# Kernel optimization log

Hardware: AMD Instinct MI355X
Metric: run time of the kernel (lower is better)

## Reference

```python
import jax, jax.numpy as jnp
import numpy as np

K = 512
H = 8
B = 8
T = 1024
EPS = 1e-5


def _layernorm(x, g, b):
    mu = jnp.mean(x, axis=-1, keepdims=True)
    var = jnp.var(x, axis=-1, keepdims=True)
    return (x - mu) * jax.lax.rsqrt(var + EPS) * g + b


def _attention(x, enc, wq, wk, wv, wo):
    b, t, k = x.shape
    h = H
    scale = k ** (-0.25)
    q = (x @ wq).reshape(b, t, h, k) * scale        # [b,t,h,k]
    kk = (enc @ wk).reshape(b, t, h, k) * scale
    v = (enc @ wv).reshape(b, t, h, k)
    dot = jnp.einsum('bqhd,bkhd->bhqk', q, kk)      # [b,h,t,t]
    att = jax.nn.softmax(dot, axis=-1)
    out = jnp.einsum('bhqk,bkhd->bqhd', att, v).reshape(b, t, h * k)
    return out @ wo                                  # [b,t,k]


def setup_inputs() -> dict:
    key = jax.random.key(0)
    ks = jax.random.split(key, 12)
    s = 0.02
    return {
        'x': jax.random.normal(ks[0], (B, T, K), jnp.float32),
        'enc': jax.random.normal(ks[1], (B, T, K), jnp.float32),
        'sa_wq': jax.random.normal(ks[2], (K, K * H), jnp.float32) * s,
        'sa_wk': jax.random.normal(ks[3], (K, K * H), jnp.float32) * s,
        'sa_wv': jax.random.normal(ks[4], (K, K * H), jnp.float32) * s,
        'sa_wo': jax.random.normal(ks[5], (K * H, K), jnp.float32) * s,
        'ca_wq': jax.random.normal(ks[6], (K, K * H), jnp.float32) * s,
        'ca_wk': jax.random.normal(ks[7], (K, K * H), jnp.float32) * s,
        'ca_wv': jax.random.normal(ks[8], (K, K * H), jnp.float32) * s,
        'ca_wo': jax.random.normal(ks[9], (K * H, K), jnp.float32) * s,
        'ln1_g': jnp.ones((K,), jnp.float32), 'ln1_b': jnp.zeros((K,), jnp.float32),
        'ln2_g': jnp.ones((K,), jnp.float32), 'ln2_b': jnp.zeros((K,), jnp.float32),
        'ln3_g': jnp.ones((K,), jnp.float32), 'ln3_b': jnp.zeros((K,), jnp.float32),
        'ff_w1': jax.random.normal(ks[10], (K, 4 * K), jnp.float32) * s,
        'ff_b1': jnp.zeros((4 * K,), jnp.float32),
        'ff_w2': jax.random.normal(ks[11], (4 * K, K), jnp.float32) * s,
        'ff_b2': jnp.zeros((K,), jnp.float32),
    }


def reference(x, enc, sa_wq, sa_wk, sa_wv, sa_wo, ca_wq, ca_wk, ca_wv, ca_wo,
              ln1_g, ln1_b, ln2_g, ln2_b, ln3_g, ln3_b,
              ff_w1, ff_b1, ff_w2, ff_b2):
    # masked self-attention (mask_future_steps=False -> plain self-attn)
    sa = _attention(x, x, sa_wq, sa_wk, sa_wv, sa_wo)
    x = _layernorm(sa + x, ln1_g, ln1_b)
    # encoder-decoder attention
    ca = _attention(x, enc, ca_wq, ca_wk, ca_wv, ca_wo)
    x = _layernorm(ca + x, ln2_g, ln2_b)
    # dropout p=0.0 -> identity
    ff = jax.nn.relu(x @ ff_w1 + ff_b1) @ ff_w2 + ff_b2
    x = _layernorm(ff + x, ln3_g, ln3_b)
    return x
```

## Files before the change

kernel.cpp:

```cpp
#include <hip/hip_runtime.h>
#include <stdint.h>

typedef short short8 __attribute__((ext_vector_type(8)));
typedef float f32x4 __attribute__((ext_vector_type(4)));
typedef unsigned short us4 __attribute__((ext_vector_type(4)));

#define DEVI static __device__ __forceinline__

DEVI float b2f(unsigned short u) {
  union { float f; uint32_t i; } v; v.i = ((uint32_t)u) << 16; return v.f;
}
DEVI unsigned short f2b(float f) {
  union { float f; uint32_t i; } v; v.f = f;
  uint32_t r = v.i + 0x7FFFu + ((v.i >> 16) & 1u);
  return (unsigned short)(r >> 16);
}

DEVI void async_cp16(const unsigned short* g, unsigned short* l) {
  __builtin_amdgcn_global_load_lds(
      (const __attribute__((address_space(1))) void*)g,
      (__attribute__((address_space(3))) void*)l, 16, 0, 0);
}

DEVI void swz(int& bx, int& by, int& bz) {
  const int gx = gridDim.x, gy = gridDim.y, gz = gridDim.z;
  int l = blockIdx.x + gx * (blockIdx.y + gy * blockIdx.z);
  bz = l % gz; l /= gz;
  by = l % gy;
  bx = l / gy;
}


__global__ __launch_bounds__(256) void cvt_f32_bf16(
    const float4* __restrict__ src, unsigned short* __restrict__ dst) {
  const int i = blockIdx.x * 256 + threadIdx.x;
  float4 f = src[i];
  uint2 o;
  o.x = (uint32_t)f2b(f.x) | ((uint32_t)f2b(f.y) << 16);
  o.y = (uint32_t)f2b(f.z) | ((uint32_t)f2b(f.w) << 16);
  ((uint2*)dst)[i] = o;
}

__global__ __launch_bounds__(256) void wtrans(
    const float* __restrict__ src, unsigned short* __restrict__ dst, int R, int C) {
  __shared__ float tile[32][33];
  const int tx = threadIdx.x & 31, ty = threadIdx.x >> 5;
  const int c0 = blockIdx.x * 32, r0 = blockIdx.y * 32;
#pragma unroll
  for (int i = 0; i < 32; i += 8)
    tile[ty + i][tx] = src[(long)(r0 + ty + i) * C + c0 + tx];
  __syncthreads();
#pragma unroll
  for (int i = 0; i < 32; i += 8)
    dst[(long)(c0 + ty + i) * R + r0 + tx] = f2b(tile[tx][ty + i]);
}

__global__ __launch_bounds__(256) void layernorm_rows(
    const float* X, const float* __restrict__ g,
    const float* __restrict__ b, float* Y,
    unsigned short* __restrict__ Yb) {
  const int tid = threadIdx.x;
  const long row = blockIdx.x;
  const float* x = X + row * 512;
  float v0 = x[tid], v1 = x[tid + 256];
  float s1 = v0 + v1;
  float s2 = v0 * v0 + v1 * v1;
#pragma unroll
  for (int o = 1; o < 64; o <<= 1) {
    s1 += __shfl_xor(s1, o);
    s2 += __shfl_xor(s2, o);
  }
  __shared__ float r1[4], r2[4];
  const int lane = tid & 63, wave = tid >> 6;
  if (lane == 0) { r1[wave] = s1; r2[wave] = s2; }
  __syncthreads();
  s1 = r1[0] + r1[1] + r1[2] + r1[3];
  s2 = r2[0] + r2[1] + r2[2] + r2[3];
  const float mu = s1 * (1.f / 512.f);
  const float var = s2 * (1.f / 512.f) - mu * mu;
  const float rs = rsqrtf(var + 1e-5f);
  float y0 = (v0 - mu) * rs * g[tid] + b[tid];
  float y1 = (v1 - mu) * rs * g[tid + 256] + b[tid + 256];
  if (Y) { Y[row * 512 + tid] = y0; Y[row * 512 + tid + 256] = y1; }
  if (Yb) { Yb[row * 512 + tid] = f2b(y0); Yb[row * 512 + tid + 256] = f2b(y1); }
}

template <int EPI, int BM, int BK, int SMAX = 0>
__global__ __launch_bounds__(256, 2) void gemm_bt(
    const unsigned short* __restrict__ A, int lda, long asb, long ash,
    const unsigned short* __restrict__ B, int ldb, long bsb, long bsh,
    void* Cv, int ldc, long csb, long csh,
    int K, float scale,
    const float* __restrict__ bias, const float* res) {
  constexpr int MI = BM / 32;
  constexpr int KS = BK / 32;
  constexpr int CPR = BK / 8;
  constexpr int SWM = CPR - 1;
  constexpr int RPL = (BK >= 64) ? 1 : (64 / BK);
  static_assert(!SMAX || (BM == 128 && EPI == 0), "SMAX: BM=128, EPI=0 only");
  __shared__ __align__(16) unsigned short As[2][BM * BK];
  __shared__ __align__(16) unsigned short Bs[2][128 * BK];
  __shared__ float inv_s[SMAX ? 128 : 1];
  int bx, by, bz;
  swz(bx, by, bz);
  const int tid = threadIdx.x;
  const int lane = tid & 63;
  const int wave = tid >> 6;
  const int zb = bz >> 3, zh = bz & 7;
  const int m0 = by * BM;
  const int n0 = bx * 128;

  const unsigned short* Ab = A + zb * asb + zh * ash + (long)m0 * lda;
  const unsigned short* Bb = B + zb * bsb + zh * bsh + (long)n0 * ldb;

  if constexpr (SMAX) {
    unsigned short* Sp = (unsigned short*)Ab;
    const int g16 = tid & 15;
#pragma unroll
    for (int p = 0; p < 8; p++) {
      const int r = p * 16 + (tid >> 4);
      us4* rowp = (us4*)(Sp + (long)r * lda);
      us4 raw[16];
#pragma unroll
      for (int c = 0; c < 16; c++) raw[c] = rowp[g16 + c * 16];
      float m = -3.0e38f;
#pragma unroll
      for (int c = 0; c < 16; c++)
#pragma unroll
        for (int e = 0; e < 4; e++) m = fmaxf(m, b2f(raw[c][e]));
#pragma unroll
      for (int o = 1; o < 16; o <<= 1) m = fmaxf(m, __shfl_xor(m, o));
      float s = 0.f;
#pragma unroll
      for (int c = 0; c < 16; c++) {
        us4 outv;
#pragma unroll
        for (int e = 0; e < 4; e++) {
          const float ev = __expf(b2f(raw[c][e]) - m);
          s += ev;
          outv[e] = f2b(ev);
        }
        raw[c] = outv;
      }
#pragma unroll
      for (int o = 1; o < 16; o <<= 1) s += __shfl_xor(s, o);
      if (g16 == 0) inv_s[r] = 1.f / s;
#pragma unroll
      for (int c = 0; c < 16; c++) rowp[g16 + c * 16] = raw[c];
    }
    __syncthreads();
  }

  f32x4 acc[MI][4];
#pragma unroll
  for (int i = 0; i < MI; i++)
#pragma unroll
    for (int j = 0; j < 4; j++) acc[i][j] = (f32x4){0.f, 0.f, 0.f, 0.f};

  const int wm = (wave >> 1) * (BM / 2);
  const int wn = (wave & 1) << 6;
  const int fm = lane & 15;
  const int kq = lane >> 4;

  auto stage_region = [&](unsigned short* Ls, const unsigned short* Gb,
                          int ld, int kt, int nch) {
#pragma unroll
    for (int c = 0; c < nch / 256; c++) {
      const int idx = c * 256 + tid;
      const int row = idx / CPR, slot = idx % CPR;
      const int col = ((slot ^ ((row / RPL) & SWM)) << 3);
      async_cp16(Gb + (long)row * ld + kt + col, Ls + idx * 8);
    }
  };
  auto stage = [&](int buf, int kt) {
    stage_region(As[buf], Ab, lda, kt, BM * CPR);
    stage_region(Bs[buf], Bb, ldb, kt, 128 * CPR);
  };
  auto sidx = [&](int row, int kc) {
    return row * BK + ((kc ^ ((row / RPL) & SWM)) << 3);
  };

  const int nt = K / BK;
  stage(0, 0);
  __syncthreads();
  int cur = 0;
  for (int t = 0; t < nt; ++t) {
    if (t + 1 < nt) stage(cur ^ 1, (t + 1) * BK);

    short8 af[MI][KS], bfr[4][KS];
#pragma unroll
    for (int ks = 0; ks < KS; ks++) {
#pragma unroll
      for (int i = 0; i < MI; i++)
        af[i][ks] = *(const short8*)&As[cur][sidx(wm + i * 16 + fm, ks * 4 + kq)];
#pragma unroll
      for (int j = 0; j < 4; j++)
        bfr[j][ks] = *(const short8*)&Bs[cur][sidx(wn + j * 16 + fm, ks * 4 + kq)];
    }
#pragma unroll
    for (int ks = 0; ks < KS; ks++)
#pragma unroll
      for (int i = 0; i < MI; i++)
#pragma unroll
        for (int j = 0; j < 4; j++)
          acc[i][j] = __builtin_amdgcn_mfma_f32_16x16x32_bf16(
              af[i][ks], bfr[j][ks], acc[i][j], 0, 0, 0);

    __syncthreads();
    cur ^= 1;
  }

  const long coff = zb * csb + zh * csh;
  const int er = (lane >> 4) << 2;
  const int ec = lane & 15;
#pragma unroll
  for (int i = 0; i < MI; i++) {
#pragma unroll
    for (int j = 0; j < 4; j++) {
      const int gc = n0 + wn + j * 16 + ec;
#pragma unroll
      for (int r = 0; r < 4; r++) {
        const int gr = m0 + wm + i * 16 + er + r;
        const float v = acc[i][j][r];
        const long idx = coff + (long)gr * ldc + gc;
        if constexpr (EPI == 0) {
          float sc = scale;
          if constexpr (SMAX) sc = inv_s[wm + i * 16 + er + r];
          ((unsigned short*)Cv)[idx] = f2b(v * sc);
        } else if constexpr (EPI == 1) {
          float o = v;
          if (bias) o += bias[gc];
          if (res) o += res[(long)gr * ldc + gc];
          ((float*)Cv)[idx] = o;
        } else {
          ((unsigned short*)Cv)[idx] = f2b(fmaxf(v + bias[gc], 0.f));
        }
      }
    }
  }
}

extern "C" void kernel_launch(void* const* d_in, const int* in_sizes, int n_in,
                              void* d_out, int out_size, void* d_ws, size_t ws_size,
                              hipStream_t stream) {
  const float* x     = (const float*)d_in[0];
  const float* enc   = (const float*)d_in[1];
  const float* ln1_g = (const float*)d_in[10];
  const float* ln1_b = (const float*)d_in[11];
  const float* ln2_g = (const float*)d_in[12];
  const float* ln2_b = (const float*)d_in[13];
  const float* ln3_g = (const float*)d_in[14];
  const float* ln3_b = (const float*)d_in[15];
  const float* ff_b1 = (const float*)d_in[17];
  const float* ff_b2 = (const float*)d_in[19];

  uint8_t* ws = (uint8_t*)d_ws;
  auto US = [&](size_t o) { return (unsigned short*)(ws + o); };
  auto F  = [&](size_t o) { return (float*)(ws + o); };

  const size_t MB = 1ull << 20;
  const size_t SZ_WBIG = 4 * MB, SZ_WFF = 2 * MB;

  const size_t O_XB = 0, O_ENCB = 8 * MB, O_WT = 16 * MB;
  const size_t O_RES = 52 * MB;
  const size_t O_XNB = 68 * MB;
  auto WT = [&](int i) { return US(O_WT + (size_t)i * SZ_WBIG); };

  int HP = 1;
  for (int c = 8; c >= 1; c >>= 1)
    if (ws_size >= (76 + 40 * (size_t)c) * MB) { HP = c; break; }
  const int NG = 8 / HP;
  const int NZ = HP * 8;
  const int LD = HP * 512;
  const size_t O_QG  = 76 * MB;
  const size_t O_KG  = O_QG + (size_t)HP * 8 * MB;
  const size_t O_VTG = O_KG + (size_t)HP * 8 * MB;
  const size_t O_SG  = O_VTG + (size_t)HP * 8 * MB;
  const size_t O_H   = 76 * MB;

  const float qsc = 0.21022410381342863f;
  dim3 B256(256);

  cvt_f32_bf16<<<4096, B256, 0, stream>>>((const float4*)x, US(O_XB));
  cvt_f32_bf16<<<4096, B256, 0, stream>>>((const float4*)enc, US(O_ENCB));

  struct WSpec { const float* s; size_t off; int R, C; };
  const WSpec wspec[10] = {
      {(const float*)d_in[2], O_WT + 0 * SZ_WBIG, 512, 4096},
      {(const float*)d_in[3], O_WT + 1 * SZ_WBIG, 512, 4096},
      {(const float*)d_in[4], O_WT + 2 * SZ_WBIG, 512, 4096},
      {(const float*)d_in[5], O_WT + 3 * SZ_WBIG, 4096, 512},
      {(const float*)d_in[6], O_WT + 4 * SZ_WBIG, 512, 4096},
      {(const float*)d_in[7], O_WT + 5 * SZ_WBIG, 512, 4096},
      {(const float*)d_in[8], O_WT + 6 * SZ_WBIG, 512, 4096},
      {(const float*)d_in[9], O_WT + 7 * SZ_WBIG, 4096, 512},
      {(const float*)d_in[16], O_WT + 8 * SZ_WBIG, 512, 2048},
      {(const float*)d_in[18], O_WT + 8 * SZ_WBIG + SZ_WFF, 2048, 512},
  };
  for (int i = 0; i < 10; i++)
    wtrans<<<dim3(wspec[i].C / 32, wspec[i].R / 32), B256, 0, stream>>>(
        wspec[i].s, US(wspec[i].off), wspec[i].R, wspec[i].C);

  auto attention = [&](const unsigned short* qsrc, const unsigned short* kvsrc,
                       int wb, const float* resid) {
    for (int g = 0; g < NG; g++) {
      const size_t woff = (size_t)g * LD * 512;
      gemm_bt<0, 128, 32><<<dim3(HP * 4, 64, 1), B256, 0, stream>>>(
          qsrc, 512, 0, 0, WT(wb + 0) + woff, 512, 0, 0,
          US(O_QG), LD, 0, 0, 512, qsc, nullptr, nullptr);
      gemm_bt<0, 128, 32><<<dim3(HP * 4, 64, 1), B256, 0, stream>>>(
          kvsrc, 512, 0, 0, WT(wb + 1) + woff, 512, 0, 0,
          US(O_KG), LD, 0, 0, 512, qsc, nullptr, nullptr);
      gemm_bt<0, 128, 32><<<dim3(64, HP * 4, 1), B256, 0, stream>>>(
          WT(wb + 2) + woff, 512, 0, 0, kvsrc, 512, 0, 0,
          US(O_VTG), 8192, 0, 0, 512, 1.f, nullptr, nullptr);
      gemm_bt<0, 128, 32><<<dim3(8, 8, NZ), B256, 0, stream>>>(
          US(O_QG), LD, 512L, (long)1024 * LD,
          US(O_KG), LD, 512L, (long)1024 * LD,
          US(O_SG), 1024, 8388608L, 1048576L, 512, 1.f, nullptr, nullptr);
      gemm_bt<0, 128, 32, 1><<<dim3(4, 8, NZ), B256, 0, stream>>>(
          US(O_SG), 1024, 8388608L, 1048576L,
          US(O_VTG), 8192, 4194304L, 1024L,
          US(O_QG), LD, 512L, (long)1024 * LD, 1024, 1.f, nullptr, nullptr);
      gemm_bt<1, 64, 64><<<dim3(4, 128, 1), B256, 0, stream>>>(
          US(O_QG), LD, 0, 0, WT(wb + 3) + (size_t)g * LD, 4096, 0, 0,
          F(O_RES), 512, 0, 0, LD, 1.f, nullptr, g == 0 ? resid : F(O_RES));
    }
  };

  attention(US(O_XB), US(O_XB), 0, x);
  layernorm_rows<<<8192, B256, 0, stream>>>(F(O_RES), ln1_g, ln1_b, F(O_RES), US(O_XNB));
  attention(US(O_XNB), US(O_ENCB), 4, F(O_RES));
  layernorm_rows<<<8192, B256, 0, stream>>>(F(O_RES), ln2_g, ln2_b, F(O_RES), US(O_XNB));
  gemm_bt<2, 128, 32><<<dim3(16, 64, 1), B256, 0, stream>>>(
      US(O_XNB), 512, 0, 0, WT(8), 512, 0, 0,
      US(O_H), 2048, 0, 0, 512, 1.f, ff_b1, nullptr);
  gemm_bt<1, 64, 64><<<dim3(4, 128, 1), B256, 0, stream>>>(
      US(O_H), 2048, 0, 0, US(O_WT + 8 * SZ_WBIG + SZ_WFF), 2048, 0, 0,
      F(O_RES), 512, 0, 0, 2048, 1.f, ff_b2, F(O_RES));
  layernorm_rows<<<8192, B256, 0, stream>>>(F(O_RES), ln3_g, ln3_b, (float*)d_out, nullptr);
}
```

Baseline: 1.405 ms.

## Fuse softmax exponent and row sums into QK^T epilogue, normalize in PV

The in-place softmax prologue in the PV GEMM is removed. Each PV block used to re-read, exponentiate and rewrite its 128 score rows, and four column blocks repeated that on the same rows. Now the QK^T GEMM epilogue writes exp(score) directly and atomically adds per-row partial sums into a zeroed scratch buffer, and the PV epilogue divides by the row sum. The max subtraction is dropped, so large logits could overflow. The output buffer is borrowed as scratch for the row sums, and an extra zeroing kernel and atomics are added per group.

Result: faster. 1.161 ms (-17.4%).

```diff
diff --git a/kernel.cpp b/kernel.cpp
--- a/kernel.cpp
+++ b/kernel.cpp
@@ -3,7 +3,6 @@
 
 typedef short short8 __attribute__((ext_vector_type(8)));
 typedef float f32x4 __attribute__((ext_vector_type(4)));
-typedef unsigned short us4 __attribute__((ext_vector_type(4)));
 
 #define DEVI static __device__ __forceinline__
 
@@ -39,6 +38,10 @@
   o.x = (uint32_t)f2b(f.x) | ((uint32_t)f2b(f.y) << 16);
   o.y = (uint32_t)f2b(f.z) | ((uint32_t)f2b(f.w) << 16);
   ((uint2*)dst)[i] = o;
+}
+
+__global__ __launch_bounds__(256) void zero_f32(float4* __restrict__ p) {
+  p[blockIdx.x * 256 + threadIdx.x] = (float4){0.f, 0.f, 0.f, 0.f};
 }
 
 __global__ __launch_bounds__(256) void wtrans(
@@ -85,7 +88,7 @@
   if (Yb) { Yb[row * 512 + tid] = f2b(y0); Yb[row * 512 + tid + 256] = f2b(y1); }
 }
 
-template <int EPI, int BM, int BK, int SMAX = 0>
+template <int EPI, int BM, int BK>
 __global__ __launch_bounds__(256, 2) void gemm_bt(
     const unsigned short* __restrict__ A, int lda, long asb, long ash,
     const unsigned short* __restrict__ B, int ldb, long bsb, long bsh,
@@ -97,10 +100,8 @@
   constexpr int CPR = BK / 8;
   constexpr int SWM = CPR - 1;
   constexpr int RPL = (BK >= 64) ? 1 : (64 / BK);
-  static_assert(!SMAX || (BM == 128 && EPI == 0), "SMAX: BM=128, EPI=0 only");
   __shared__ __align__(16) unsigned short As[2][BM * BK];
   __shared__ __align__(16) unsigned short Bs[2][128 * BK];
-  __shared__ float inv_s[SMAX ? 128 : 1];
   int bx, by, bz;
   swz(bx, by, bz);
   const int tid = threadIdx.x;
@@ -113,44 +114,6 @@
   const unsigned short* Ab = A + zb * asb + zh * ash + (long)m0 * lda;
   const unsigned short* Bb = B + zb * bsb + zh * bsh + (long)n0 * ldb;
 
-  if constexpr (SMAX) {
-    unsigned short* Sp = (unsigned short*)Ab;
-    const int g16 = tid & 15;
-#pragma unroll
-    for (int p = 0; p < 8; p++) {
-      const int r = p * 16 + (tid >> 4);
-      us4* rowp = (us4*)(Sp + (long)r * lda);
-      us4 raw[16];
-#pragma unroll
-      for (int c = 0; c < 16; c++) raw[c] = rowp[g16 + c * 16];
-      float m = -3.0e38f;
-#pragma unroll
-      for (int c = 0; c < 16; c++)
-#pragma unroll
-        for (int e = 0; e < 4; e++) m = fmaxf(m, b2f(raw[c][e]));
-#pragma unroll
-      for (int o = 1; o < 16; o <<= 1) m = fmaxf(m, __shfl_xor(m, o));
-      float s = 0.f;
-#pragma unroll
-      for (int c = 0; c < 16; c++) {
-        us4 outv;
-#pragma unroll
-        for (int e = 0; e < 4; e++) {
-          const float ev = __expf(b2f(raw[c][e]) - m);
-          s += ev;
-          outv[e] = f2b(ev);
-        }
-        raw[c] = outv;
-      }
-#pragma unroll
-      for (int o = 1; o < 16; o <<= 1) s += __shfl_xor(s, o);
-      if (g16 == 0) inv_s[r] = 1.f / s;
-#pragma unroll
-      for (int c = 0; c < 16; c++) rowp[g16 + c * 16] = raw[c];
-    }
-    __syncthreads();
-  }
-
   f32x4 acc[MI][4];
 #pragma unroll
   for (int i = 0; i < MI; i++)
@@ -213,27 +176,63 @@
   const long coff = zb * csb + zh * csh;
   const int er = (lane >> 4) << 2;
   const int ec = lane & 15;
-#pragma unroll
-  for (int i = 0; i < MI; i++) {
-#pragma unroll
-    for (int j = 0; j < 4; j++) {
-      const int gc = n0 + wn + j * 16 + ec;
+
+  if constexpr (EPI == 5) {
+    float* rowsum = const_cast<float*>(res);
+#pragma unroll
+    for (int i = 0; i < MI; i++) {
 #pragma unroll
       for (int r = 0; r < 4; r++) {
         const int gr = m0 + wm + i * 16 + er + r;
-        const float v = acc[i][j][r];
-        const long idx = coff + (long)gr * ldc + gc;
-        if constexpr (EPI == 0) {
-          float sc = scale;
-          if constexpr (SMAX) sc = inv_s[wm + i * 16 + er + r];
-          ((unsigned short*)Cv)[idx] = f2b(v * sc);
-        } else if constexpr (EPI == 1) {
-          float o = v;
-          if (bias) o += bias[gc];
-          if (res) o += res[(long)gr * ldc + gc];
-          ((float*)Cv)[idx] = o;
-        } else {
-          ((unsigned short*)Cv)[idx] = f2b(fmaxf(v + bias[gc], 0.f));
+        float part = 0.f;
+#pragma unroll
+        for (int j = 0; j < 4; j++) {
+          const int gc = n0 + wn + j * 16 + ec;
+          const float e = __expf(acc[i][j][r]);
+          part += e;
+          ((unsigned short*)Cv)[coff + (long)gr * ldc + gc] = f2b(e);
+        }
+#pragma unroll
+        for (int o = 1; o < 16; o <<= 1) part += __shfl_xor(part, o);
+        if (ec == 0) atomicAdd(&rowsum[(long)bz * 1024 + gr], part);
+      }
+    }
+  } else if constexpr (EPI == 4) {
+#pragma unroll
+    for (int i = 0; i < MI; i++) {
+#pragma unroll
+      for (int r = 0; r < 4; r++) {
+        const int gr = m0 + wm + i * 16 + er + r;
+        const float inv = 1.f / res[(long)bz * 1024 + gr];
+#pragma unroll
+        for (int j = 0; j < 4; j++) {
+          const int gc = n0 + wn + j * 16 + ec;
+          ((unsigned short*)Cv)[coff + (long)gr * ldc + gc] =
+              f2b(acc[i][j][r] * inv);
+        }
+      }
+    }
+  } else {
+#pragma unroll
+    for (int i = 0; i < MI; i++) {
+#pragma unroll
+      for (int j = 0; j < 4; j++) {
+        const int gc = n0 + wn + j * 16 + ec;
+#pragma unroll
+        for (int r = 0; r < 4; r++) {
+          const int gr = m0 + wm + i * 16 + er + r;
+          const float v = acc[i][j][r];
+          const long idx = coff + (long)gr * ldc + gc;
+          if constexpr (EPI == 0) {
+            ((unsigned short*)Cv)[idx] = f2b(v * scale);
+          } else if constexpr (EPI == 1) {
+            float o = v;
+            if (bias) o += bias[gc];
+            if (res) o += res[(long)gr * ldc + gc];
+            ((float*)Cv)[idx] = o;
+          } else {
+            ((unsigned short*)Cv)[idx] = f2b(fmaxf(v + bias[gc], 0.f));
+          }
         }
       }
     }
@@ -278,6 +277,8 @@
   const size_t O_SG  = O_VTG + (size_t)HP * 8 * MB;
   const size_t O_H   = 76 * MB;
 
+  float* rowsum = (float*)d_out;
+
   const float qsc = 0.21022410381342863f;
   dim3 B256(256);
 
@@ -314,14 +315,15 @@
       gemm_bt<0, 128, 32><<<dim3(64, HP * 4, 1), B256, 0, stream>>>(
           WT(wb + 2) + woff, 512, 0, 0, kvsrc, 512, 0, 0,
           US(O_VTG), 8192, 0, 0, 512, 1.f, nullptr, nullptr);
-      gemm_bt<0, 128, 32><<<dim3(8, 8, NZ), B256, 0, stream>>>(
+      zero_f32<<<NZ, B256, 0, stream>>>((float4*)rowsum);
+      gemm_bt<5, 128, 32><<<dim3(8, 8, NZ), B256, 0, stream>>>(
           US(O_QG), LD, 512L, (long)1024 * LD,
           US(O_KG), LD, 512L, (long)1024 * LD,
-          US(O_SG), 1024, 8388608L, 1048576L, 512, 1.f, nullptr, nullptr);
-      gemm_bt<0, 128, 32, 1><<<dim3(4, 8, NZ), B256, 0, stream>>>(
+          US(O_SG), 1024, 8388608L, 1048576L, 512, 1.f, nullptr, rowsum);
+      gemm_bt<4, 128, 32><<<dim3(4, 8, NZ), B256, 0, stream>>>(
           US(O_SG), 1024, 8388608L, 1048576L,
           US(O_VTG), 8192, 4194304L, 1024L,
-          US(O_QG), LD, 512L, (long)1024 * LD, 1024, 1.f, nullptr, nullptr);
+          US(O_QG), LD, 512L, (long)1024 * LD, 1024, 1.f, nullptr, rowsum);
       gemm_bt<1, 64, 64><<<dim3(4, 128, 1), B256, 0, stream>>>(
           US(O_QG), LD, 0, 0, WT(wb + 3) + (size_t)g * LD, 4096, 0, 0,
           F(O_RES), 512, 0, 0, LD, 1.f, nullptr, g == 0 ? resid : F(O_RES));
```
